# Kernel optimization log

Measured on AMD Instinct MI355X. Metric: run time of the kernel, lower is better.

The kernel has to match this reference:

```python
import jax, jax.numpy as jnp
import numpy as np

B, S, H = 1, 2048, 2048
NH, NKV, HD = 32, 8, 64
GROUPS = NH // NKV
KV_DIM = NKV * HD
COMP = int(S * 0.5)
FF = 5632  # round_up(2048*4*2/3, 256), fla GatedMLP convention
DEPTH = 2
EPS = 1e-6


def rmsnorm(x, w):
    var = jnp.mean(jnp.square(x), axis=-1, keepdims=True)
    return x * jax.lax.rsqrt(var + EPS) * w


def setup_inputs() -> dict:
    key = jax.random.key(0)
    ks = jax.random.split(key, 10)
    sc = 0.02
    return {
        "hidden_states": jax.random.normal(ks[0], (B, S, H), jnp.float32),
        "comp_w": jax.random.normal(ks[1], (COMP, S), jnp.float32) * sc,
        "comp_b": jnp.zeros((COMP,), jnp.float32),
        "q_w": jax.random.normal(ks[2], (H, H), jnp.float32) * sc,
        "k_w": jax.random.normal(ks[3], (KV_DIM, H), jnp.float32) * sc,
        "v_w": jax.random.normal(ks[4], (KV_DIM, H), jnp.float32) * sc,
        "o_w": jax.random.normal(ks[5], (H, H), jnp.float32) * sc,
        "attn_norm_w": jnp.ones((H,), jnp.float32),
        "mlp_norm_w": jnp.ones((H,), jnp.float32),
        "gate_w": jax.random.normal(ks[6], (FF, H), jnp.float32) * sc,
        "up_w": jax.random.normal(ks[7], (FF, H), jnp.float32) * sc,
        "down_w": jax.random.normal(ks[8], (H, FF), jnp.float32) * sc,
    }


def reference(hidden_states, comp_w, comp_b, q_w, k_w, v_w, o_w,
              attn_norm_w, mlp_norm_w, gate_w, up_w, down_w):
    # init_compressed_tokens: Linear over the sequence axis
    # (b,s,h) -> transpose -> (b,h,s) @ W^T -> (b,h,c) -> transpose -> (b,c,h)
    compressed = jnp.einsum('bsh,cs->bch', hidden_states, comp_w) + comp_b[None, :, None]

    for _ in range(DEPTH):
        residual = jnp.concatenate([hidden_states, compressed], axis=1)  # (b, s+c, h)
        ct = rmsnorm(compressed, attn_norm_w)
        q = (ct @ q_w.T).reshape(B, COMP, NH, HD)
        k = (residual @ k_w.T).reshape(B, S + COMP, NKV, HD)
        v = (residual @ v_w.T).reshape(B, S + COMP, NKV, HD)
        # GQA expand (repeat_interleave along head dim)
        k = jnp.repeat(k, GROUPS, axis=2)
        v = jnp.repeat(v, GROUPS, axis=2)
        scores = jnp.einsum('bsnk,btnk->bsnt', q, k) / (HD ** 0.5)
        attn = jax.nn.softmax(scores, axis=-1)
        o = jnp.einsum('bsnt,btnk->bsnk', attn, v).reshape(B, COMP, H)
        compressed = o @ o_w.T + ct
        ct2 = rmsnorm(compressed, mlp_norm_w)
        mlp_out = (jax.nn.silu(ct2 @ gate_w.T) * (ct2 @ up_w.T)) @ down_w.T
        compressed = mlp_out + ct2
    return compressed
```

## Files before the change

### kernel.cpp

```cpp
#include <hip/hip_runtime.h>
#include <math.h>

constexpr int S_   = 2048;
constexpr int H_   = 2048;
constexpr int NH_  = 32;
constexpr int NKV_ = 8;
constexpr int HD_  = 64;
constexpr int GROUPS_ = NH_ / NKV_;
constexpr int KV_  = NKV_ * HD_;
constexpr int KV2_ = 2 * KV_;
constexpr int COMP_ = 1024;
constexpr int FF_  = 5632;
constexpr int GU2_ = 2 * FF_;
constexpr int TOT_ = S_ + COMP_;
constexpr float EPS_ = 1e-6f;
constexpr int SK_ = 4;
constexpr int SP_ = 2;
constexpr float LOG2E_ = 1.44269504088896340736f;

typedef __attribute__((ext_vector_type(4))) float f32x4;
typedef __attribute__((ext_vector_type(8))) short bf16x8;
typedef __attribute__((ext_vector_type(8))) ushort u16x8;

__device__ __forceinline__ ushort f2bf(float x) {
    union { float f; unsigned u; } v; v.f = x;
    unsigned r = v.u + 0x7fffu + ((v.u >> 16) & 1u);
    return (ushort)(r >> 16);
}
__device__ __forceinline__ float bf2f(ushort x) {
    union { unsigned u; float f; } v; v.u = ((unsigned)x) << 16;
    return v.f;
}
__device__ __forceinline__ uint cvtpk_bf16(float lo, float hi) {
    uint r;
    asm("v_cvt_pk_bf16_f32 %0, %1, %2" : "=v"(r) : "v"(lo), "v"(hi));
    return r;
}

__global__ __launch_bounds__(256) void f2b_k(
    const float* __restrict__ x, ushort* __restrict__ y, int n4)
{
    int i = blockIdx.x * 256 + threadIdx.x;
    const int stride = gridDim.x * 256;
    for (; i < n4; i += stride) {
        float4 v = ((const float4*)x)[i];
        ushort4 r = {f2bf(v.x), f2bf(v.y), f2bf(v.z), f2bf(v.w)};
        ((ushort4*)y)[i] = r;
    }
}

__global__ __launch_bounds__(256) void tpose64(
    const ushort* __restrict__ in, ushort* __restrict__ out,
    int R, int C, int ldi)
{
    __shared__ ushort T[64][72];
    const int r0 = blockIdx.x * 64, c0 = blockIdx.y * 64;
    const int row = threadIdx.x >> 2, seg = threadIdx.x & 3;

    const ushort* g = &in[(size_t)(r0 + row) * ldi + c0 + seg * 16];
    *(u16x8*)&T[row][seg * 16]     = *(const u16x8*)g;
    *(u16x8*)&T[row][seg * 16 + 8] = *(const u16x8*)(g + 8);
    __syncthreads();

    ushort tmp[16];
#pragma unroll
    for (int j = 0; j < 16; j++) tmp[j] = T[seg * 16 + j][row];
    ushort* go = &out[(size_t)(c0 + row) * R + r0 + seg * 16];
    *(u16x8*)go       = *(const u16x8*)&tmp[0];
    *(u16x8*)(go + 8) = *(const u16x8*)&tmp[8];
}

__global__ __launch_bounds__(256) void mfma_gemm(
    const ushort* __restrict__ A, const ushort* __restrict__ B,
    const float* __restrict__ addp, const float* __restrict__ bias,
    float oscale, float* __restrict__ outf, ushort* __restrict__ outb,
    int M, int N, int K)
{
    __shared__ ushort Alds[128 * 32];
    __shared__ ushort Blds[128 * 32];

    const int tid  = threadIdx.x;
    const int w    = tid >> 6;
    const int lane = tid & 63;
    const int bm = blockIdx.y, bn = blockIdx.x;
    const int wr = w >> 1, wc = w & 1;
    const int fr = lane & 15;
    const int fq = lane >> 4;
    const int srow = lane >> 2;
    const int skof = (lane & 3) * 8;

    f32x4 acc[4][4];
#pragma unroll
    for (int i = 0; i < 4; i++)
#pragma unroll
        for (int j = 0; j < 4; j++)
            acc[i][j] = (f32x4){0.f, 0.f, 0.f, 0.f};

    for (int k0 = 0; k0 < K; k0 += 32) {
        __syncthreads();
#pragma unroll
        for (int i = 0; i < 2; i++) {
            const int slot = w * 2 + i;
            const ushort* ga = &A[(size_t)(bm * 128 + slot * 16 + srow) * K + k0 + skof];
            __builtin_amdgcn_global_load_lds(
                (const __attribute__((address_space(1))) void*)ga,
                (__attribute__((address_space(3))) void*)&Alds[slot * 512], 16, 0, 0);
            const ushort* gb = &B[(size_t)(bn * 128 + slot * 16 + srow) * K + k0 + skof];
            __builtin_amdgcn_global_load_lds(
                (const __attribute__((address_space(1))) void*)gb,
                (__attribute__((address_space(3))) void*)&Blds[slot * 512], 16, 0, 0);
        }
        __syncthreads();

        bf16x8 a[4], b[4];
#pragma unroll
        for (int mt = 0; mt < 4; mt++)
            a[mt] = *(const bf16x8*)&Alds[(wr * 64 + mt * 16 + fr) * 32 + fq * 8];
#pragma unroll
        for (int nt = 0; nt < 4; nt++)
            b[nt] = *(const bf16x8*)&Blds[(wc * 64 + nt * 16 + fr) * 32 + fq * 8];

#pragma unroll
        for (int mt = 0; mt < 4; mt++)
#pragma unroll
            for (int nt = 0; nt < 4; nt++)
                acc[mt][nt] = __builtin_amdgcn_mfma_f32_16x16x32_bf16(
                    a[mt], b[nt], acc[mt][nt], 0, 0, 0);
    }

#pragma unroll
    for (int mt = 0; mt < 4; mt++) {
#pragma unroll
        for (int nt = 0; nt < 4; nt++) {
#pragma unroll
            for (int r = 0; r < 4; r++) {
                const int row = bm * 128 + wr * 64 + mt * 16 + fq * 4 + r;
                const int col = bn * 128 + wc * 64 + nt * 16 + fr;
                float v = acc[mt][nt][r] * oscale;
                if (bias) v += bias[row];
                if (addp) v += addp[(size_t)row * N + col];
                if (outf) outf[(size_t)row * N + col] = v;
                if (outb) outb[(size_t)row * N + col] = f2bf(v);
            }
        }
    }
}

#define BARS do { __builtin_amdgcn_s_barrier(); __builtin_amdgcn_sched_barrier(0); } while (0)
#define VMW(n) asm volatile("s_waitcnt vmcnt(" #n ")" ::: "memory")
#define STG(gp, lp) __builtin_amdgcn_global_load_lds( \
    (const __attribute__((address_space(1))) void*)(gp), \
    (__attribute__((address_space(3))) void*)(lp), 16, 0, 0)
#define STA(bufA, R0, kt) STG(Ag + (size_t)(R0) * K + (kt) * 64, &(bufA)[((R0) + w * 8) * 64])
#define STB(bufB, R0, kt) STG(Bg + (size_t)(R0) * K + (kt) * 64, &(bufB)[((R0) + w * 8) * 64])

__device__ __forceinline__ void ldaq(bf16x8 (&aa)[2][2], const ushort* bufA,
                                     int m0, int aoff, int s0, int s1)
{
#pragma unroll
    for (int m = 0; m < 2; m++) {
        aa[m][0] = *(const bf16x8*)&bufA[aoff + (m0 + m) * 1024 + s0];
        aa[m][1] = *(const bf16x8*)&bufA[aoff + (m0 + m) * 1024 + s1];
    }
}
__device__ __forceinline__ void ldbq(bf16x8 (&bb)[4][2], const ushort* bufB,
                                     int boff, int s0, int s1)
{
#pragma unroll
    for (int nt = 0; nt < 4; nt++) {
        bb[nt][0] = *(const bf16x8*)&bufB[boff + nt * 1024 + s0];
        bb[nt][1] = *(const bf16x8*)&bufB[boff + nt * 1024 + s1];
    }
}
template <int M0>
__device__ __forceinline__ void mfmaq(f32x4 (&acc)[8][4], bf16x8 (&aa)[2][2],
                                      bf16x8 (&bb)[4][2])
{
    __builtin_amdgcn_s_setprio(1);
#pragma unroll
    for (int m = 0; m < 2; m++)
#pragma unroll
        for (int nt = 0; nt < 4; nt++) {
            acc[M0 + m][nt] = __builtin_amdgcn_mfma_f32_16x16x32_bf16(
                aa[m][0], bb[nt][0], acc[M0 + m][nt], 0, 0, 0);
            acc[M0 + m][nt] = __builtin_amdgcn_mfma_f32_16x16x32_bf16(
                aa[m][1], bb[nt][1], acc[M0 + m][nt], 0, 0, 0);
        }
    __builtin_amdgcn_s_setprio(0);
}

__global__ __launch_bounds__(512, 2) void gemm8ph(
    const ushort* __restrict__ A, const ushort* __restrict__ B,
    ushort* __restrict__ C, int N, int K)
{
    alignas(16) __shared__ ushort lds[4][16384];
    ushort* const lA0 = lds[0];
    ushort* const lB0 = lds[1];
    ushort* const lA1 = lds[2];
    ushort* const lB1 = lds[3];

    const int tid = threadIdx.x;
    const int w = tid >> 6, lane = tid & 63;
    const int wr = w >> 2, wc = w & 3;
    const int fr = lane & 15, fq = lane >> 4;
    const int xk = fr & 7;

    const int nwg = gridDim.x;
    const int nbn = N >> 8;
    int id = (int)blockIdx.x;
    if (!(nwg & 7)) id = (id & 7) * (nwg >> 3) + (id >> 3);
    const int bm = id / nbn, bn = id - bm * nbn;

    const int srow = lane >> 3;
    const int scol = ((lane & 7) ^ srow) << 3;
    const ushort* Ag = A + (size_t)(bm * 256 + w * 8 + srow) * K + scol;
    const ushort* Bg = B + (size_t)(bn * 256 + w * 8 + srow) * K + scol;

    const int aoff = (wr * 128 + fr) * 64;
    const int boff = (wc * 64 + fr) * 64;
    const int s0 = ((0 + fq) ^ xk) << 3;
    const int s1 = ((4 + fq) ^ xk) << 3;

    f32x4 acc[8][4];
#pragma unroll
    for (int i = 0; i < 8; i++)
#pragma unroll
        for (int j = 0; j < 4; j++) acc[i][j] = (f32x4){0.f, 0.f, 0.f, 0.f};

    bf16x8 aa[2][2], bb[4][2];

    STB(lB0, 0, 0);   STB(lB0, 64, 0);
    STA(lA0, 0, 0);   STA(lA0, 128, 0);
    STB(lB0, 128, 0); STB(lB0, 192, 0);
    STA(lA0, 64, 0);  STA(lA0, 192, 0);
    STB(lB1, 0, 1);   STB(lB1, 64, 1);
    STA(lA1, 0, 1);   STA(lA1, 128, 1);
    STB(lB1, 128, 1); STB(lB1, 192, 1);
    VMW(6);
    BARS;

    const int NITER = K >> 7;
    for (int i = 0; i < NITER - 1; i++) {
        const int t1 = 2 * i + 1, t2 = 2 * i + 2, t3 = 2 * i + 3;
        ldbq(bb, lB0, boff, s0, s1);
        ldaq(aa, lA0, 0, aoff, s0, s1);
        STA(lA1, 64, t1); STA(lA1, 192, t1);
        BARS; mfmaq<0>(acc, aa, bb); BARS;
        ldaq(aa, lA0, 2, aoff, s0, s1);
        STB(lB0, 0, t2); STB(lB0, 64, t2);
        BARS; mfmaq<2>(acc, aa, bb); BARS;
        ldaq(aa, lA0, 4, aoff, s0, s1);
        STA(lA0, 0, t2); STA(lA0, 128, t2);
        BARS; mfmaq<4>(acc, aa, bb); BARS;
        ldaq(aa, lA0, 6, aoff, s0, s1);
        STB(lB0, 128, t2); STB(lB0, 192, t2);
        BARS; mfmaq<6>(acc, aa, bb); VMW(6); BARS;
        ldbq(bb, lB1, boff, s0, s1);
        ldaq(aa, lA1, 0, aoff, s0, s1);
        STA(lA0, 64, t2); STA(lA0, 192, t2);
        BARS; mfmaq<0>(acc, aa, bb); BARS;
        ldaq(aa, lA1, 2, aoff, s0, s1);
        STB(lB1, 0, t3); STB(lB1, 64, t3);
        BARS; mfmaq<2>(acc, aa, bb); BARS;
        ldaq(aa, lA1, 4, aoff, s0, s1);
        STA(lA1, 0, t3); STA(lA1, 128, t3);
        BARS; mfmaq<4>(acc, aa, bb); BARS;
        ldaq(aa, lA1, 6, aoff, s0, s1);
        STB(lB1, 128, t3); STB(lB1, 192, t3);
        BARS; mfmaq<6>(acc, aa, bb); VMW(6); BARS;
    }
    {
        const int t1 = 2 * NITER - 1;
        ldbq(bb, lB0, boff, s0, s1);
        ldaq(aa, lA0, 0, aoff, s0, s1);
        STA(lA1, 64, t1); STA(lA1, 192, t1);
        BARS; mfmaq<0>(acc, aa, bb); BARS;
        ldaq(aa, lA0, 2, aoff, s0, s1);
        BARS; mfmaq<2>(acc, aa, bb); BARS;
        ldaq(aa, lA0, 4, aoff, s0, s1);
        BARS; mfmaq<4>(acc, aa, bb); BARS;
        ldaq(aa, lA0, 6, aoff, s0, s1);
        BARS; mfmaq<6>(acc, aa, bb); VMW(0); BARS;
        ldbq(bb, lB1, boff, s0, s1);
        ldaq(aa, lA1, 0, aoff, s0, s1);
        BARS; mfmaq<0>(acc, aa, bb); BARS;
        ldaq(aa, lA1, 2, aoff, s0, s1);
        BARS; mfmaq<2>(acc, aa, bb); BARS;
        ldaq(aa, lA1, 4, aoff, s0, s1);
        BARS; mfmaq<4>(acc, aa, bb); BARS;
        ldaq(aa, lA1, 6, aoff, s0, s1);
        mfmaq<6>(acc, aa, bb);
    }

    ushort* Cb = C + (size_t)(bm * 256 + wr * 128 + fq * 4) * N
                   + bn * 256 + wc * 64 + fr;
#pragma unroll
    for (int mt = 0; mt < 8; mt++)
#pragma unroll
        for (int nt = 0; nt < 4; nt++)
#pragma unroll
            for (int r = 0; r < 4; r++)
                Cb[(size_t)(mt * 16 + r) * N + nt * 16] = f2bf(acc[mt][nt][r]);
}

__global__ __launch_bounds__(256) void mfma_gemm_sk(
    const ushort* __restrict__ A, const ushort* __restrict__ B,
    float* __restrict__ part, int M, int N, int K, int Kc)
{
    __shared__ ushort Alds[128 * 32];
    __shared__ ushort Blds[128 * 32];

    const int tid  = threadIdx.x;
    const int w    = tid >> 6;
    const int lane = tid & 63;
    const int bm = blockIdx.y, bn = blockIdx.x, z = blockIdx.z;
    const int wr = w >> 1, wc = w & 1;
    const int fr = lane & 15;
    const int fq = lane >> 4;
    const int srow = lane >> 2;
    const int skof = (lane & 3) * 8;

    f32x4 acc[4][4];
#pragma unroll
    for (int i = 0; i < 4; i++)
#pragma unroll
        for (int j = 0; j < 4; j++)
            acc[i][j] = (f32x4){0.f, 0.f, 0.f, 0.f};

    const int kbeg = z * Kc;
    for (int k0 = kbeg; k0 < kbeg + Kc; k0 += 32) {
        __syncthreads();
#pragma unroll
        for (int i = 0; i < 2; i++) {
            const int slot = w * 2 + i;
            const ushort* ga = &A[(size_t)(bm * 128 + slot * 16 + srow) * K + k0 + skof];
            __builtin_amdgcn_global_load_lds(
                (const __attribute__((address_space(1))) void*)ga,
                (__attribute__((address_space(3))) void*)&Alds[slot * 512], 16, 0, 0);
            const ushort* gb = &B[(size_t)(bn * 128 + slot * 16 + srow) * K + k0 + skof];
            __builtin_amdgcn_global_load_lds(
                (const __attribute__((address_space(1))) void*)gb,
                (__attribute__((address_space(3))) void*)&Blds[slot * 512], 16, 0, 0);
        }
        __syncthreads();

        bf16x8 a[4], b[4];
#pragma unroll
        for (int mt = 0; mt < 4; mt++)
            a[mt] = *(const bf16x8*)&Alds[(wr * 64 + mt * 16 + fr) * 32 + fq * 8];
#pragma unroll
        for (int nt = 0; nt < 4; nt++)
            b[nt] = *(const bf16x8*)&Blds[(wc * 64 + nt * 16 + fr) * 32 + fq * 8];

#pragma unroll
        for (int mt = 0; mt < 4; mt++)
#pragma unroll
            for (int nt = 0; nt < 4; nt++)
                acc[mt][nt] = __builtin_amdgcn_mfma_f32_16x16x32_bf16(
                    a[mt], b[nt], acc[mt][nt], 0, 0, 0);
    }

    float* pz = part + (size_t)z * M * N;
#pragma unroll
    for (int mt = 0; mt < 4; mt++)
#pragma unroll
        for (int nt = 0; nt < 4; nt++)
#pragma unroll
            for (int r = 0; r < 4; r++) {
                const int row = bm * 128 + wr * 64 + mt * 16 + fq * 4 + r;
                const int col = bn * 128 + wc * 64 + nt * 16 + fr;
                pz[(size_t)row * N + col] = acc[mt][nt][r];
            }
}

__global__ __launch_bounds__(256) void sk_reduce(
    const float* __restrict__ part, int mn4, int n4,
    const float* __restrict__ bias, const float* __restrict__ addp,
    float oscale, float* __restrict__ outf, ushort* __restrict__ outb)
{
    const size_t mn = (size_t)mn4 * 4;
    int i = blockIdx.x * 256 + threadIdx.x;
    const int stride = gridDim.x * 256;
    for (; i < mn4; i += stride) {
        float4 v = ((const float4*)part)[i];
#pragma unroll
        for (int z = 1; z < SK_; z++) {
            const float4 pz = ((const float4*)(part + z * mn))[i];
            v.x += pz.x; v.y += pz.y; v.z += pz.z; v.w += pz.w;
        }
        v.x *= oscale; v.y *= oscale; v.z *= oscale; v.w *= oscale;
        if (bias) {
            const float bb = bias[i / n4];
            v.x += bb; v.y += bb; v.z += bb; v.w += bb;
        }
        if (addp) {
            const float4 ad = ((const float4*)addp)[i];
            v.x += ad.x; v.y += ad.y; v.z += ad.z; v.w += ad.w;
        }
        if (outf) ((float4*)outf)[i] = v;
        if (outb) {
            ushort4 r = {f2bf(v.x), f2bf(v.y), f2bf(v.z), f2bf(v.w)};
            ((ushort4*)outb)[i] = r;
        }
    }
}

__global__ __launch_bounds__(256) void attn_mfma(
    const ushort* __restrict__ q, const ushort* __restrict__ k, int ldk,
    const ushort* __restrict__ vt, float* __restrict__ attp,
    float* __restrict__ ml)
{
    constexpr int KSPAN = TOT_ / SP_;
    alignas(16) __shared__ ushort Kb[2][8 * 512];
    alignas(16) __shared__ ushort Vb[2][8 * 512];
    alignas(16) __shared__ ushort Ps[64 * 64];

    const int qt = blockIdx.x, h = blockIdx.y, z = blockIdx.z;
    const int kvh = h / GROUPS_;
    const int tid = threadIdx.x;
    const int w = tid >> 6, lane = tid & 63;
    const int fr = lane & 15, fq = lane >> 4;
    const int q0 = qt * 64;

    const ushort* qrow = &q[(size_t)(q0 + w * 16 + fr) * H_ + h * HD_];
    const bf16x8 bq0 = *(const bf16x8*)(qrow + fq * 8);
    const bf16x8 bq1 = *(const bf16x8*)(qrow + 32 + fq * 8);

    float m = -1e30f, l = 0.f;
    f32x4 acc[4];
#pragma unroll
    for (int nt = 0; nt < 4; nt++) acc[nt] = (f32x4){0.f, 0.f, 0.f, 0.f};

    const int t_beg = z * KSPAN;
    const ushort* kp = &k[(size_t)(t_beg + w * 16 + fr) * ldk + kvh * HD_ + fq * 8];
    const ushort* vp = &vt[(size_t)(kvh * HD_ + w * 16 + fr) * TOT_ + t_beg + fq * 8];

#define ASTG(gp, lp) __builtin_amdgcn_global_load_lds( \
    (const __attribute__((address_space(1))) void*)(gp), \
    (__attribute__((address_space(3))) void*)(lp), 16, 0, 0)

    ASTG(kp,      &Kb[0][w * 512]);
    ASTG(kp + 32, &Kb[0][(4 + w) * 512]);
    ASTG(vp,      &Vb[0][w * 512]);
    ASTG(vp + 32, &Vb[0][(4 + w) * 512]);
    asm volatile("s_waitcnt vmcnt(0)" ::: "memory");
    __syncthreads();
    const ushort* kn = kp + (size_t)64 * ldk;
    const ushort* vn = vp + 64;

    const int pxor = (fr & 7) << 4;
    char* const psb = (char*)&Ps[(w * 16 + fr) * 64];

    const int NT = KSPAN / 64;
    int cur = 0;
    for (int t = 0; t < NT; t++) {
        f32x4 st[4];
        __builtin_amdgcn_s_setprio(1);
#pragma unroll
        for (int nt = 0; nt < 4; nt++) {
            const bf16x8 a0 = *(const bf16x8*)&Kb[cur][(nt * 64 + lane) * 8];
            const bf16x8 a1 = *(const bf16x8*)&Kb[cur][((4 + nt) * 64 + lane) * 8];
            f32x4 tacc = (f32x4){0.f, 0.f, 0.f, 0.f};
            tacc = __builtin_amdgcn_mfma_f32_16x16x32_bf16(a0, bq0, tacc, 0, 0, 0);
            tacc = __builtin_amdgcn_mfma_f32_16x16x32_bf16(a1, bq1, tacc, 0, 0, 0);
            st[nt] = tacc;
        }
        __builtin_amdgcn_s_setprio(0);

        if (t + 1 < NT) {
            ASTG(kn,      &Kb[cur ^ 1][w * 512]);
            ASTG(kn + 32, &Kb[cur ^ 1][(4 + w) * 512]);
            ASTG(vn,      &Vb[cur ^ 1][w * 512]);
            ASTG(vn + 32, &Vb[cur ^ 1][(4 + w) * 512]);
            kn += (size_t)64 * ldk;
            vn += 64;
        }

        float mt = st[0][0];
#pragma unroll
        for (int nt = 0; nt < 4; nt++)
#pragma unroll
            for (int r = 0; r < 4; r++) mt = fmaxf(mt, st[nt][r]);
        mt = fmaxf(mt, __shfl_xor(mt, 16));
        mt = fmaxf(mt, __shfl_xor(mt, 32));
        if (!__all(mt <= m + 8.0f)) {
            const float mnew = fmaxf(m, mt);
            const float alpha = exp2f(m - mnew);
            m = mnew;
            l *= alpha;
            const float ar0 = __shfl(alpha, fq * 4 + 0, 16);
            const float ar1 = __shfl(alpha, fq * 4 + 1, 16);
            const float ar2 = __shfl(alpha, fq * 4 + 2, 16);
            const float ar3 = __shfl(alpha, fq * 4 + 3, 16);
#pragma unroll
            for (int nt = 0; nt < 4; nt++) {
                acc[nt][0] *= ar0; acc[nt][1] *= ar1;
                acc[nt][2] *= ar2; acc[nt][3] *= ar3;
            }
        }
        float ss = 0.f;
#pragma unroll
        for (int nt = 0; nt < 4; nt++)
#pragma unroll
            for (int r = 0; r < 4; r++) {
                const float pv = exp2f(st[nt][r] - m);
                st[nt][r] = pv;
                ss += pv;
            }
        ss += __shfl_xor(ss, 16);
        ss += __shfl_xor(ss, 32);
        l += ss;

#pragma unroll
        for (int nt = 0; nt < 4; nt++) {
            uint2 uu;
            uu.x = cvtpk_bf16(st[nt][0], st[nt][1]);
            uu.y = cvtpk_bf16(st[nt][2], st[nt][3]);
            *(uint2*)(psb + ((nt * 32 + fq * 8) ^ pxor)) = uu;
        }
        const bf16x8 ap0 = *(const bf16x8*)(psb + ((fq * 16) ^ pxor));
        const bf16x8 ap1 = *(const bf16x8*)(psb + ((64 + fq * 16) ^ pxor));

        __builtin_amdgcn_s_setprio(1);
#pragma unroll
        for (int nt = 0; nt < 4; nt++) {
            const bf16x8 b0 = *(const bf16x8*)&Vb[cur][(nt * 64 + lane) * 8];
            const bf16x8 b1 = *(const bf16x8*)&Vb[cur][((4 + nt) * 64 + lane) * 8];
            acc[nt] = __builtin_amdgcn_mfma_f32_16x16x32_bf16(ap0, b0, acc[nt], 0, 0, 0);
            acc[nt] = __builtin_amdgcn_mfma_f32_16x16x32_bf16(ap1, b1, acc[nt], 0, 0, 0);
        }
        __builtin_amdgcn_s_setprio(0);

        asm volatile("s_waitcnt vmcnt(0)" ::: "memory");
        __syncthreads();
        cur ^= 1;
    }
#undef ASTG

    float* pz = attp + (size_t)z * COMP_ * H_;
#pragma unroll
    for (int r = 0; r < 4; r++) {
        const int row = q0 + w * 16 + fq * 4 + r;
#pragma unroll
        for (int nt = 0; nt < 4; nt++)
            pz[(size_t)row * H_ + h * HD_ + nt * 16 + fr] = acc[nt][r];
    }
    if (lane < 16)
        ((float2*)ml)[((size_t)z * NH_ + h) * COMP_ + (q0 + w * 16 + fr)] =
            make_float2(m, l);
}

__global__ __launch_bounds__(256) void attn_merge(
    const float* __restrict__ attp, const float* __restrict__ ml,
    ushort* __restrict__ o, int n4)
{
    constexpr int H4 = H_ / 4;
    constexpr size_t PS = (size_t)COMP_ * H_;
    int i = blockIdx.x * 256 + threadIdx.x;
    const int stride = gridDim.x * 256;
    for (; i < n4; i += stride) {
        const int row = i / H4;
        const int col = (i - row * H4) * 4;
        const int h = col >> 6;
        const float2 ml0 = ((const float2*)ml)[((size_t)0 * NH_ + h) * COMP_ + row];
        const float2 ml1 = ((const float2*)ml)[((size_t)1 * NH_ + h) * COMP_ + row];
        const float M = fmaxf(ml0.x, ml1.x);
        const float a0 = exp2f(ml0.x - M), a1 = exp2f(ml1.x - M);
        const float inv = 1.0f / (a0 * ml0.y + a1 * ml1.y);
        const float4 p0 = ((const float4*)attp)[i];
        const float4 p1 = ((const float4*)(attp + PS))[i];
        ushort4 r = {f2bf((a0 * p0.x + a1 * p1.x) * inv),
                     f2bf((a0 * p0.y + a1 * p1.y) * inv),
                     f2bf((a0 * p0.z + a1 * p1.z) * inv),
                     f2bf((a0 * p0.w + a1 * p1.w) * inv)};
        ((ushort4*)o)[i] = r;
    }
}

__global__ __launch_bounds__(256) void rmsnorm_dual_k(
    const float* __restrict__ x, const float* __restrict__ w,
    float* __restrict__ y, ushort* __restrict__ yb)
{
    const int row = blockIdx.x;
    const float* xr = x + (size_t)row * H_;
    __shared__ float red[256];

    float s = 0.f;
#pragma unroll
    for (int i = 0; i < 8; i++) {
        const float v = xr[threadIdx.x + i * 256];
        s += v * v;
    }
    red[threadIdx.x] = s;
    __syncthreads();
    for (int t = 128; t > 0; t >>= 1) {
        if (threadIdx.x < t) red[threadIdx.x] += red[threadIdx.x + t];
        __syncthreads();
    }
    const float scale = rsqrtf(red[0] * (1.0f / H_) + EPS_);
#pragma unroll
    for (int i = 0; i < 8; i++) {
        const int idx = threadIdx.x + i * 256;
        const float v = xr[idx] * scale * w[idx];
        y[(size_t)row * H_ + idx] = v;
        yb[(size_t)row * H_ + idx] = f2bf(v);
    }
}

__global__ __launch_bounds__(256) void silu_mul_gu(
    const ushort* __restrict__ gu, ushort* __restrict__ g, int n4)
{
    constexpr int FF4 = FF_ / 4;
    int i = blockIdx.x * 256 + threadIdx.x;
    const int stride = gridDim.x * 256;
    for (; i < n4; i += stride) {
        const int row = i / FF4;
        const int c = (i - row * FF4) * 4;
        ushort4 gv = *(const ushort4*)&gu[(size_t)row * GU2_ + c];
        ushort4 uv = *(const ushort4*)&gu[(size_t)row * GU2_ + FF_ + c];
        float x0 = bf2f(gv.x), x1 = bf2f(gv.y), x2 = bf2f(gv.z), x3 = bf2f(gv.w);
        x0 = x0 / (1.f + __expf(-x0)) * bf2f(uv.x);
        x1 = x1 / (1.f + __expf(-x1)) * bf2f(uv.y);
        x2 = x2 / (1.f + __expf(-x2)) * bf2f(uv.z);
        x3 = x3 / (1.f + __expf(-x3)) * bf2f(uv.w);
        ushort4 r = {f2bf(x0), f2bf(x1), f2bf(x2), f2bf(x3)};
        ((ushort4*)g)[i] = r;
    }
}

extern "C" void kernel_launch(void* const* d_in, const int* in_sizes, int n_in,
                              void* d_out, int out_size, void* d_ws, size_t ws_size,
                              hipStream_t stream)
{
    (void)in_sizes; (void)n_in; (void)out_size; (void)ws_size;

    const float* hidden      = (const float*)d_in[0];
    const float* comp_w      = (const float*)d_in[1];
    const float* comp_b      = (const float*)d_in[2];
    const float* q_w         = (const float*)d_in[3];
    const float* k_w         = (const float*)d_in[4];
    const float* v_w         = (const float*)d_in[5];
    const float* o_w         = (const float*)d_in[6];
    const float* attn_norm_w = (const float*)d_in[7];
    const float* mlp_norm_w  = (const float*)d_in[8];
    const float* gate_w      = (const float*)d_in[9];
    const float* up_w        = (const float*)d_in[10];
    const float* down_w      = (const float*)d_in[11];
    float* out = (float*)d_out;

    char* p = (char*)d_ws;
    auto alloc = [&](size_t bytes) -> char* {
        char* r = p; p += (bytes + 255) & ~(size_t)255; return r;
    };
    ushort* qw_bf    = (ushort*)alloc((size_t)H_ * H_ * 2);
    ushort* kvw_bf   = (ushort*)alloc((size_t)KV2_ * H_ * 2);
    ushort* ow_bf    = (ushort*)alloc((size_t)H_ * H_ * 2);
    ushort* guw_bf   = (ushort*)alloc((size_t)GU2_ * H_ * 2);
    ushort* down_bf  = (ushort*)alloc((size_t)H_ * FF_ * 2);
    ushort* compw_bf = (ushort*)alloc((size_t)COMP_ * S_ * 2);
    ushort* hidcomp  = (ushort*)alloc((size_t)TOT_ * H_ * 2);
    ushort* hidT     = (ushort*)alloc((size_t)H_ * S_ * 2);
    ushort* ct_bf    = (ushort*)alloc((size_t)COMP_ * H_ * 2);
    ushort* ct2_bf   = (ushort*)alloc((size_t)COMP_ * H_ * 2);
    ushort* ob_bf    = (ushort*)alloc((size_t)COMP_ * H_ * 2);
    ushort* qb_bf    = (ushort*)alloc((size_t)COMP_ * H_ * 2);
    ushort* kvb_bf   = (ushort*)alloc((size_t)TOT_ * KV2_ * 2);
    ushort* vt_bf    = (ushort*)alloc((size_t)KV_ * TOT_ * 2);
    ushort* gb_bf    = (ushort*)alloc((size_t)COMP_ * FF_ * 2);
    float* comp0 = (float*)alloc((size_t)COMP_ * H_ * 4);
    float* comp1 = (float*)alloc((size_t)COMP_ * H_ * 4);
    float* ct    = (float*)alloc((size_t)COMP_ * H_ * 4);
    float* ct2   = (float*)alloc((size_t)COMP_ * H_ * 4);
    float*  skbuf = (float*)alloc((size_t)SK_ * TOT_ * KV2_ * 4);
    ushort* gub   = (ushort*)skbuf;
    float*  attp  = skbuf;
    float*  mlbuf = skbuf + (size_t)SP_ * COMP_ * H_;

    ushort* cur_bf = hidcomp + (size_t)S_ * H_;

    const dim3 blk(256);

    f2b_k<<<512, blk, 0, stream>>>(q_w,    qw_bf,            H_ * H_ / 4);
    f2b_k<<<512, blk, 0, stream>>>(k_w,    kvw_bf,           KV_ * H_ / 4);
    f2b_k<<<512, blk, 0, stream>>>(v_w,    kvw_bf + (size_t)KV_ * H_, KV_ * H_ / 4);
    f2b_k<<<512, blk, 0, stream>>>(o_w,    ow_bf,            H_ * H_ / 4);
    f2b_k<<<512, blk, 0, stream>>>(gate_w, guw_bf,           FF_ * H_ / 4);
    f2b_k<<<512, blk, 0, stream>>>(up_w,   guw_bf + (size_t)FF_ * H_, FF_ * H_ / 4);
    f2b_k<<<512, blk, 0, stream>>>(down_w, down_bf,          H_ * FF_ / 4);
    f2b_k<<<512, blk, 0, stream>>>(comp_w, compw_bf,         COMP_ * S_ / 4);
    f2b_k<<<512, blk, 0, stream>>>(hidden, hidcomp,          S_ * H_ / 4);
    tpose64<<<dim3(S_ / 64, H_ / 64), blk, 0, stream>>>(hidcomp, hidT, S_, H_, H_);

    mfma_gemm_sk<<<dim3(H_ / 128, COMP_ / 128, SK_), blk, 0, stream>>>(
        compw_bf, hidT, skbuf, COMP_, H_, S_, S_ / SK_);
    sk_reduce<<<1024, blk, 0, stream>>>(
        skbuf, COMP_ * H_ / 4, H_ / 4, comp_b, nullptr, 1.f, comp0, cur_bf);

    float* cur = comp0;
    for (int d = 0; d < 2; d++) {
        rmsnorm_dual_k<<<COMP_, blk, 0, stream>>>(cur, attn_norm_w, ct, ct_bf);

        mfma_gemm_sk<<<dim3(H_ / 128, COMP_ / 128, SK_), blk, 0, stream>>>(
            ct_bf, qw_bf, skbuf, COMP_, H_, H_, H_ / SK_);
        sk_reduce<<<1024, blk, 0, stream>>>(
            skbuf, COMP_ * H_ / 4, H_ / 4, nullptr, nullptr, 0.125f * LOG2E_,
            nullptr, qb_bf);

        mfma_gemm_sk<<<dim3(KV2_ / 128, TOT_ / 128, SK_), blk, 0, stream>>>(
            hidcomp, kvw_bf, skbuf, TOT_, KV2_, H_, H_ / SK_);
        sk_reduce<<<1024, blk, 0, stream>>>(
            skbuf, TOT_ * KV2_ / 4, KV2_ / 4, nullptr, nullptr, 1.f, nullptr, kvb_bf);

        tpose64<<<dim3(TOT_ / 64, KV_ / 64), blk, 0, stream>>>(
            kvb_bf + KV_, vt_bf, TOT_, KV_, KV2_);

        attn_mfma<<<dim3(COMP_ / 64, NH_, SP_), blk, 0, stream>>>(
            qb_bf, kvb_bf, KV2_, vt_bf, attp, mlbuf);
        attn_merge<<<512, blk, 0, stream>>>(attp, mlbuf, ob_bf, COMP_ * H_ / 4);

        mfma_gemm_sk<<<dim3(H_ / 128, COMP_ / 128, SK_), blk, 0, stream>>>(
            ob_bf, ow_bf, skbuf, COMP_, H_, H_, H_ / SK_);
        sk_reduce<<<1024, blk, 0, stream>>>(
            skbuf, COMP_ * H_ / 4, H_ / 4, nullptr, ct, 1.f, comp1, nullptr);

        rmsnorm_dual_k<<<COMP_, blk, 0, stream>>>(comp1, mlp_norm_w, ct2, ct2_bf);

        gemm8ph<<<dim3((GU2_ / 256) * (COMP_ / 256)), dim3(512), 0, stream>>>(
            ct2_bf, guw_bf, gub, GU2_, H_);

        silu_mul_gu<<<1024, blk, 0, stream>>>(gub, gb_bf, COMP_ * FF_ / 4);

        float* dst = (d == 1) ? out : comp0;
        ushort* dst_bf = (d == 1) ? nullptr : cur_bf;
        mfma_gemm_sk<<<dim3(H_ / 128, COMP_ / 128, SK_), blk, 0, stream>>>(
            gb_bf, down_bf, skbuf, COMP_, H_, FF_, FF_ / SK_);
        sk_reduce<<<1024, blk, 0, stream>>>(
            skbuf, COMP_ * H_ / 4, H_ / 4, nullptr, ct2, 1.f, dst, dst_bf);
        cur = dst;
    }
}
```

Baseline: 887.6 us.

## Fuse SiLU-mul into gate/up GEMM epilogue and RMSNorm into split-K reduce

Gate and up weights are interleaved in 16-row blocks during the bf16 conversion, so each gate/up GEMM tile holds matching gate and up columns. SiLU(gate)*up is then computed in the epilogue and written straight to the bf16 activation, which removes the intermediate gate/up buffer and the separate silu kernel. The split-K reduction is also fused with the residual add and RMSNorm (one block per row), which removes the standalone rmsnorm kernels and the fp32 round trips of the comp buffers. The cost is a less parallel reduction, one 256-thread block per row, and gate/up values that are no longer rounded to bf16 before the SiLU product.

```diff
diff --git a/kernel.cpp b/kernel.cpp
--- a/kernel.cpp
+++ b/kernel.cpp
@@ -49,6 +49,23 @@
     }
 }
 
+__global__ __launch_bounds__(256) void f2b_gu(
+    const float* __restrict__ gate, const float* __restrict__ up,
+    ushort* __restrict__ dst, int n4)
+{
+    constexpr int H4 = H_ / 4;
+    int i = blockIdx.x * 256 + threadIdx.x;
+    const int stride = gridDim.x * 256;
+    for (; i < n4; i += stride) {
+        const int j = i / H4, c4 = i - j * H4;
+        const float* src = ((j >> 4) & 1) ? up : gate;
+        const int srow = ((j >> 5) << 4) | (j & 15);
+        const float4 v = ((const float4*)src)[srow * H4 + c4];
+        ushort4 r = {f2bf(v.x), f2bf(v.y), f2bf(v.z), f2bf(v.w)};
+        ((ushort4*)dst)[i] = r;
+    }
+}
+
 __global__ __launch_bounds__(256) void tpose64(
     const ushort* __restrict__ in, ushort* __restrict__ out,
     int R, int C, int ldi)
@@ -68,82 +85,6 @@
     ushort* go = &out[(size_t)(c0 + row) * R + r0 + seg * 16];
     *(u16x8*)go       = *(const u16x8*)&tmp[0];
     *(u16x8*)(go + 8) = *(const u16x8*)&tmp[8];
-}
-
-__global__ __launch_bounds__(256) void mfma_gemm(
-    const ushort* __restrict__ A, const ushort* __restrict__ B,
-    const float* __restrict__ addp, const float* __restrict__ bias,
-    float oscale, float* __restrict__ outf, ushort* __restrict__ outb,
-    int M, int N, int K)
-{
-    __shared__ ushort Alds[128 * 32];
-    __shared__ ushort Blds[128 * 32];
-
-    const int tid  = threadIdx.x;
-    const int w    = tid >> 6;
-    const int lane = tid & 63;
-    const int bm = blockIdx.y, bn = blockIdx.x;
-    const int wr = w >> 1, wc = w & 1;
-    const int fr = lane & 15;
-    const int fq = lane >> 4;
-    const int srow = lane >> 2;
-    const int skof = (lane & 3) * 8;
-
-    f32x4 acc[4][4];
-#pragma unroll
-    for (int i = 0; i < 4; i++)
-#pragma unroll
-        for (int j = 0; j < 4; j++)
-            acc[i][j] = (f32x4){0.f, 0.f, 0.f, 0.f};
-
-    for (int k0 = 0; k0 < K; k0 += 32) {
-        __syncthreads();
-#pragma unroll
-        for (int i = 0; i < 2; i++) {
-            const int slot = w * 2 + i;
-            const ushort* ga = &A[(size_t)(bm * 128 + slot * 16 + srow) * K + k0 + skof];
-            __builtin_amdgcn_global_load_lds(
-                (const __attribute__((address_space(1))) void*)ga,
-                (__attribute__((address_space(3))) void*)&Alds[slot * 512], 16, 0, 0);
-            const ushort* gb = &B[(size_t)(bn * 128 + slot * 16 + srow) * K + k0 + skof];
-            __builtin_amdgcn_global_load_lds(
-                (const __attribute__((address_space(1))) void*)gb,
-                (__attribute__((address_space(3))) void*)&Blds[slot * 512], 16, 0, 0);
-        }
-        __syncthreads();
-
-        bf16x8 a[4], b[4];
-#pragma unroll
-        for (int mt = 0; mt < 4; mt++)
-            a[mt] = *(const bf16x8*)&Alds[(wr * 64 + mt * 16 + fr) * 32 + fq * 8];
-#pragma unroll
-        for (int nt = 0; nt < 4; nt++)
-            b[nt] = *(const bf16x8*)&Blds[(wc * 64 + nt * 16 + fr) * 32 + fq * 8];
-
-#pragma unroll
-        for (int mt = 0; mt < 4; mt++)
-#pragma unroll
-            for (int nt = 0; nt < 4; nt++)
-                acc[mt][nt] = __builtin_amdgcn_mfma_f32_16x16x32_bf16(
-                    a[mt], b[nt], acc[mt][nt], 0, 0, 0);
-    }
-
-#pragma unroll
-    for (int mt = 0; mt < 4; mt++) {
-#pragma unroll
-        for (int nt = 0; nt < 4; nt++) {
-#pragma unroll
-            for (int r = 0; r < 4; r++) {
-                const int row = bm * 128 + wr * 64 + mt * 16 + fq * 4 + r;
-                const int col = bn * 128 + wc * 64 + nt * 16 + fr;
-                float v = acc[mt][nt][r] * oscale;
-                if (bias) v += bias[row];
-                if (addp) v += addp[(size_t)row * N + col];
-                if (outf) outf[(size_t)row * N + col] = v;
-                if (outb) outb[(size_t)row * N + col] = f2bf(v);
-            }
-        }
-    }
 }
 
 #define BARS do { __builtin_amdgcn_s_barrier(); __builtin_amdgcn_sched_barrier(0); } while (0)
@@ -191,7 +132,7 @@
 
 __global__ __launch_bounds__(512, 2) void gemm8ph(
     const ushort* __restrict__ A, const ushort* __restrict__ B,
-    ushort* __restrict__ C, int N, int K)
+    ushort* __restrict__ g, int N, int K)
 {
     alignas(16) __shared__ ushort lds[4][16384];
     ushort* const lA0 = lds[0];
@@ -292,15 +233,22 @@
         mfmaq<6>(acc, aa, bb);
     }
 
-    ushort* Cb = C + (size_t)(bm * 256 + wr * 128 + fq * 4) * N
-                   + bn * 256 + wc * 64 + fr;
-#pragma unroll
-    for (int mt = 0; mt < 8; mt++)
-#pragma unroll
-        for (int nt = 0; nt < 4; nt++)
-#pragma unroll
-            for (int r = 0; r < 4; r++)
-                Cb[(size_t)(mt * 16 + r) * N + nt * 16] = f2bf(acc[mt][nt][r]);
+    const int FFo = N >> 1;
+#pragma unroll
+    for (int mt = 0; mt < 8; mt++) {
+#pragma unroll
+        for (int u = 0; u < 2; u++) {
+            const int col = (bn * 8 + wc * 2 + u) * 16 + fr;
+#pragma unroll
+            for (int r = 0; r < 4; r++) {
+                const int row = bm * 256 + wr * 128 + mt * 16 + fq * 4 + r;
+                const float xg = acc[mt][2 * u][r];
+                const float xu = acc[mt][2 * u + 1][r];
+                const float yv = xg / (1.f + __expf(-xg)) * xu;
+                g[(size_t)row * FFo + col] = f2bf(yv);
+            }
+        }
+    }
 }
 
 __global__ __launch_bounds__(256) void mfma_gemm_sk(
@@ -402,6 +350,66 @@
             ushort4 r = {f2bf(v.x), f2bf(v.y), f2bf(v.z), f2bf(v.w)};
             ((ushort4*)outb)[i] = r;
         }
+    }
+}
+
+__global__ __launch_bounds__(256) void sk_reduce_rms(
+    const float* __restrict__ part, const float* __restrict__ bias,
+    const float* __restrict__ addp, const float* __restrict__ w,
+    ushort* __restrict__ residb, float* __restrict__ y,
+    ushort* __restrict__ yb)
+{
+    constexpr size_t MN = (size_t)COMP_ * H_;
+    const int row = blockIdx.x;
+    const int t = threadIdx.x;
+    __shared__ float red[256];
+
+    float4 v[2];
+#pragma unroll
+    for (int j = 0; j < 2; j++) {
+        const int c4 = t + j * 256;
+        v[j] = ((const float4*)(part + (size_t)row * H_))[c4];
+#pragma unroll
+        for (int z = 1; z < SK_; z++) {
+            const float4 pz = ((const float4*)(part + z * MN + (size_t)row * H_))[c4];
+            v[j].x += pz.x; v[j].y += pz.y; v[j].z += pz.z; v[j].w += pz.w;
+        }
+        if (bias) {
+            const float bb = bias[row];
+            v[j].x += bb; v[j].y += bb; v[j].z += bb; v[j].w += bb;
+        }
+        if (addp) {
+            const float4 ad = ((const float4*)(addp + (size_t)row * H_))[c4];
+            v[j].x += ad.x; v[j].y += ad.y; v[j].z += ad.z; v[j].w += ad.w;
+        }
+        if (residb) {
+            ushort4 r = {f2bf(v[j].x), f2bf(v[j].y), f2bf(v[j].z), f2bf(v[j].w)};
+            ((ushort4*)(residb + (size_t)row * H_))[c4] = r;
+        }
+    }
+    float s = 0.f;
+#pragma unroll
+    for (int j = 0; j < 2; j++)
+        s += v[j].x * v[j].x + v[j].y * v[j].y + v[j].z * v[j].z + v[j].w * v[j].w;
+    red[t] = s;
+    __syncthreads();
+    for (int k = 128; k > 0; k >>= 1) {
+        if (t < k) red[t] += red[t + k];
+        __syncthreads();
+    }
+    const float scale = rsqrtf(red[0] * (1.0f / H_) + EPS_);
+#pragma unroll
+    for (int j = 0; j < 2; j++) {
+        const int c4 = t + j * 256;
+        const float4 wv = ((const float4*)w)[c4];
+        float4 nv;
+        nv.x = v[j].x * scale * wv.x;
+        nv.y = v[j].y * scale * wv.y;
+        nv.z = v[j].z * scale * wv.z;
+        nv.w = v[j].w * scale * wv.w;
+        ((float4*)(y + (size_t)row * H_))[c4] = nv;
+        ushort4 r = {f2bf(nv.x), f2bf(nv.y), f2bf(nv.z), f2bf(nv.w)};
+        ((ushort4*)(yb + (size_t)row * H_))[c4] = r;
     }
 }
 
@@ -577,57 +585,6 @@
     }
 }
 
-__global__ __launch_bounds__(256) void rmsnorm_dual_k(
-    const float* __restrict__ x, const float* __restrict__ w,
-    float* __restrict__ y, ushort* __restrict__ yb)
-{
-    const int row = blockIdx.x;
-    const float* xr = x + (size_t)row * H_;
-    __shared__ float red[256];
-
-    float s = 0.f;
-#pragma unroll
-    for (int i = 0; i < 8; i++) {
-        const float v = xr[threadIdx.x + i * 256];
-        s += v * v;
-    }
-    red[threadIdx.x] = s;
-    __syncthreads();
-    for (int t = 128; t > 0; t >>= 1) {
-        if (threadIdx.x < t) red[threadIdx.x] += red[threadIdx.x + t];
-        __syncthreads();
-    }
-    const float scale = rsqrtf(red[0] * (1.0f / H_) + EPS_);
-#pragma unroll
-    for (int i = 0; i < 8; i++) {
-        const int idx = threadIdx.x + i * 256;
-        const float v = xr[idx] * scale * w[idx];
-        y[(size_t)row * H_ + idx] = v;
-        yb[(size_t)row * H_ + idx] = f2bf(v);
-    }
-}
-
-__global__ __launch_bounds__(256) void silu_mul_gu(
-    const ushort* __restrict__ gu, ushort* __restrict__ g, int n4)
-{
-    constexpr int FF4 = FF_ / 4;
-    int i = blockIdx.x * 256 + threadIdx.x;
-    const int stride = gridDim.x * 256;
-    for (; i < n4; i += stride) {
-        const int row = i / FF4;
-        const int c = (i - row * FF4) * 4;
-        ushort4 gv = *(const ushort4*)&gu[(size_t)row * GU2_ + c];
-        ushort4 uv = *(const ushort4*)&gu[(size_t)row * GU2_ + FF_ + c];
-        float x0 = bf2f(gv.x), x1 = bf2f(gv.y), x2 = bf2f(gv.z), x3 = bf2f(gv.w);
-        x0 = x0 / (1.f + __expf(-x0)) * bf2f(uv.x);
-        x1 = x1 / (1.f + __expf(-x1)) * bf2f(uv.y);
-        x2 = x2 / (1.f + __expf(-x2)) * bf2f(uv.z);
-        x3 = x3 / (1.f + __expf(-x3)) * bf2f(uv.w);
-        ushort4 r = {f2bf(x0), f2bf(x1), f2bf(x2), f2bf(x3)};
-        ((ushort4*)g)[i] = r;
-    }
-}
-
 extern "C" void kernel_launch(void* const* d_in, const int* in_sizes, int n_in,
                               void* d_out, int out_size, void* d_ws, size_t ws_size,
                               hipStream_t stream)
@@ -667,12 +624,9 @@
     ushort* kvb_bf   = (ushort*)alloc((size_t)TOT_ * KV2_ * 2);
     ushort* vt_bf    = (ushort*)alloc((size_t)KV_ * TOT_ * 2);
     ushort* gb_bf    = (ushort*)alloc((size_t)COMP_ * FF_ * 2);
-    float* comp0 = (float*)alloc((size_t)COMP_ * H_ * 4);
-    float* comp1 = (float*)alloc((size_t)COMP_ * H_ * 4);
     float* ct    = (float*)alloc((size_t)COMP_ * H_ * 4);
     float* ct2   = (float*)alloc((size_t)COMP_ * H_ * 4);
     float*  skbuf = (float*)alloc((size_t)SK_ * TOT_ * KV2_ * 4);
-    ushort* gub   = (ushort*)skbuf;
     float*  attp  = skbuf;
     float*  mlbuf = skbuf + (size_t)SP_ * COMP_ * H_;
 
@@ -684,8 +638,7 @@
     f2b_k<<<512, blk, 0, stream>>>(k_w,    kvw_bf,           KV_ * H_ / 4);
     f2b_k<<<512, blk, 0, stream>>>(v_w,    kvw_bf + (size_t)KV_ * H_, KV_ * H_ / 4);
     f2b_k<<<512, blk, 0, stream>>>(o_w,    ow_bf,            H_ * H_ / 4);
-    f2b_k<<<512, blk, 0, stream>>>(gate_w, guw_bf,           FF_ * H_ / 4);
-    f2b_k<<<512, blk, 0, stream>>>(up_w,   guw_bf + (size_t)FF_ * H_, FF_ * H_ / 4);
+    f2b_gu<<<1024, blk, 0, stream>>>(gate_w, up_w, guw_bf,   GU2_ * H_ / 4);
     f2b_k<<<512, blk, 0, stream>>>(down_w, down_bf,          H_ * FF_ / 4);
     f2b_k<<<512, blk, 0, stream>>>(comp_w, compw_bf,         COMP_ * S_ / 4);
     f2b_k<<<512, blk, 0, stream>>>(hidden, hidcomp,          S_ * H_ / 4);
@@ -693,13 +646,10 @@
 
     mfma_gemm_sk<<<dim3(H_ / 128, COMP_ / 128, SK_), blk, 0, stream>>>(
         compw_bf, hidT, skbuf, COMP_, H_, S_, S_ / SK_);
-    sk_reduce<<<1024, blk, 0, stream>>>(
-        skbuf, COMP_ * H_ / 4, H_ / 4, comp_b, nullptr, 1.f, comp0, cur_bf);
-
-    float* cur = comp0;
+    sk_reduce_rms<<<COMP_, blk, 0, stream>>>(
+        skbuf, comp_b, nullptr, attn_norm_w, cur_bf, ct, ct_bf);
+
     for (int d = 0; d < 2; d++) {
-        rmsnorm_dual_k<<<COMP_, blk, 0, stream>>>(cur, attn_norm_w, ct, ct_bf);
-
         mfma_gemm_sk<<<dim3(H_ / 128, COMP_ / 128, SK_), blk, 0, stream>>>(
             ct_bf, qw_bf, skbuf, COMP_, H_, H_, H_ / SK_);
         sk_reduce<<<1024, blk, 0, stream>>>(
@@ -720,22 +670,20 @@
 
         mfma_gemm_sk<<<dim3(H_ / 128, COMP_ / 128, SK_), blk, 0, stream>>>(
             ob_bf, ow_bf, skbuf, COMP_, H_, H_, H_ / SK_);
-        sk_reduce<<<1024, blk, 0, stream>>>(
-            skbuf, COMP_ * H_ / 4, H_ / 4, nullptr, ct, 1.f, comp1, nullptr);
-
-        rmsnorm_dual_k<<<COMP_, blk, 0, stream>>>(comp1, mlp_norm_w, ct2, ct2_bf);
+        sk_reduce_rms<<<COMP_, blk, 0, stream>>>(
+            skbuf, nullptr, ct, mlp_norm_w, nullptr, ct2, ct2_bf);
 
         gemm8ph<<<dim3((GU2_ / 256) * (COMP_ / 256)), dim3(512), 0, stream>>>(
-            ct2_bf, guw_bf, gub, GU2_, H_);
-
-        silu_mul_gu<<<1024, blk, 0, stream>>>(gub, gb_bf, COMP_ * FF_ / 4);
-
-        float* dst = (d == 1) ? out : comp0;
-        ushort* dst_bf = (d == 1) ? nullptr : cur_bf;
+            ct2_bf, guw_bf, gb_bf, GU2_, H_);
+
         mfma_gemm_sk<<<dim3(H_ / 128, COMP_ / 128, SK_), blk, 0, stream>>>(
             gb_bf, down_bf, skbuf, COMP_, H_, FF_, FF_ / SK_);
-        sk_reduce<<<1024, blk, 0, stream>>>(
-            skbuf, COMP_ * H_ / 4, H_ / 4, nullptr, ct2, 1.f, dst, dst_bf);
-        cur = dst;
-    }
-}
+        if (d == 0) {
+            sk_reduce_rms<<<COMP_, blk, 0, stream>>>(
+                skbuf, nullptr, ct2, attn_norm_w, cur_bf, ct, ct_bf);
+        } else {
+            sk_reduce<<<1024, blk, 0, stream>>>(
+                skbuf, COMP_ * H_ / 4, H_ / 4, nullptr, ct2, 1.f, out, nullptr);
+        }
+    }
+}
```

New measurement: 833.8 us. 6.1% less time.
